# Kernel tuning notes

Hardware: AMD Instinct MI355X
Metric: run time of the kernel (lower is better)

## Reference

```python
import jax, jax.numpy as jnp
import numpy as np

K = 9          # temporal window (kernel_size)
PAD = (K - 1) // 2
BN_EPS = 1e-5


def setup_inputs() -> dict:
    key = jax.random.key(0)
    ks = jax.random.split(key, 9)
    N, Cin, Cout, T, V = 16, 64, 128, 256, 25
    return {
        "x": jax.random.normal(ks[0], (N, Cin, T, V), jnp.float32),
        "conv_w": jax.random.normal(ks[1], (Cout, Cin), jnp.float32) * (1.0 / np.sqrt(Cin)),
        "conv_b": jax.random.normal(ks[2], (Cout,), jnp.float32) * 0.01,
        "gamma": jax.random.uniform(ks[3], (Cout,), jnp.float32, 0.5, 1.5),
        "beta": jax.random.normal(ks[4], (Cout,), jnp.float32) * 0.1,
        "run_mean": jax.random.normal(ks[5], (Cout,), jnp.float32) * 0.1,
        "run_var": jax.random.uniform(ks[6], (Cout,), jnp.float32, 0.5, 1.5),
        "att0": jnp.full((1, Cout, 1, K), 1.0 / K, jnp.float32),
        "A": jax.random.uniform(ks[7], (V, V), jnp.float32),
        "keep_prob": 1,
    }


def reference(x, conv_w, conv_b, gamma, beta, run_mean, run_var, att0, A, keep_prob):
    # 1x1 conv (pointwise channel mix); AvgPool2d((1,1)) is identity for stride=1
    x = jnp.einsum("nctv,oc->notv", x, conv_w) + conv_b[None, :, None, None]
    # BatchNorm2d (eval mode: running stats)
    scale = gamma / jnp.sqrt(run_var + BN_EPS)
    x = x * scale[None, :, None, None] + (beta - run_mean * scale)[None, :, None, None]
    N, C, T, V = x.shape
    # UnfoldTemporalWindows: zero-pad T, gather K temporal shifts -> (N, C, T, K, V)
    xp = jnp.pad(x, ((0, 0), (0, 0), (PAD, PAD), (0, 0)))
    upfold = jnp.stack([xp[:, :, u:u + T, :] for u in range(K)], axis=3)
    # local attention: score each window position against the center frame
    scores = jnp.einsum("nctv,nctuv->nctu", x, upfold) / V
    attn = jax.nn.softmax(scores, axis=-1) + att0
    out = jnp.einsum("nctuv,nctu->nctv", upfold, attn)
    # dropS / dropT are identity at keep_prob == 1 (inference)
    return out
```

## Files before the change

kernel.cpp:

```cpp
#include <hip/hip_runtime.h>
#include <hip/hip_bf16.h>

#define CIN   64
#define COUT  128
#define TT    256
#define VV    25
#define TV    (TT * VV)
#define KW    9
#define PAD   4
#define RSF   32

typedef __attribute__((ext_vector_type(8))) short short8;
typedef __attribute__((ext_vector_type(4))) float f32x4;

__device__ __forceinline__ unsigned f2b(float f) {
    unsigned u = __builtin_bit_cast(unsigned, f);
    return (u + 0x7FFFu + ((u >> 16) & 1u)) >> 16;
}
__device__ __forceinline__ float b2f(unsigned short u) {
    unsigned v = (unsigned)u << 16;
    return __builtin_bit_cast(float, v);
}
__device__ __forceinline__ int swz(int row, int cbyte) {
    return row * 128 + ((cbyte & ~15) ^ ((row & 7) << 4)) + (cbyte & 15);
}
__device__ __forceinline__ int aswz(int t, int v) {
    return t * RSF + ((((v >> 2) ^ ((t >> 1) & 7))) << 2) + (v & 3);
}
__device__ __forceinline__ const float4* arow(const float* yl, int r, int k) {
    return (const float4*)&yl[r * RSF + ((k ^ ((r >> 1) & 7)) << 2)];
}

__global__ __launch_bounds__(256) void conv_mfma(
    const float* __restrict__ x, const float* __restrict__ w,
    const float* __restrict__ cb, const float* __restrict__ gamma,
    const float* __restrict__ beta, const float* __restrict__ rm,
    const float* __restrict__ rv, unsigned short* __restrict__ y)
{
    __shared__ __align__(16) unsigned short Wl[COUT * 64];
    __shared__ __align__(16) unsigned short Xl[128 * 64];
    __shared__ float sc[COUT];
    __shared__ float of[COUT];

    const int pc  = blockIdx.x;
    const int n   = blockIdx.y;
    const int tid = threadIdx.x;
    const int posbase = pc * 128;

    if (tid < COUT) {
        const float s = gamma[tid] * rsqrtf(rv[tid] + 1e-5f);
        sc[tid] = s;
        of[tid] = cb[tid] * s + beta[tid] - rm[tid] * s;
    }
    for (int idx = tid; idx < 2048; idx += 256) {
        const int c4 = idx & 15, o = idx >> 4;
        const f32x4 wv = *(const f32x4*)(w + o * 64 + c4 * 4);
        uint2 pk;
        pk.x = f2b(wv.x) | (f2b(wv.y) << 16);
        pk.y = f2b(wv.z) | (f2b(wv.w) << 16);
        *(uint2*)((char*)Wl + swz(o, c4 * 8)) = pk;
    }
    for (int idx = tid; idx < 2048; idx += 256) {
        const int pos = idx & 127, c4 = idx >> 7;
        const float* xp = x + (size_t)n * CIN * TV + (size_t)(c4 * 4) * TV + posbase + pos;
        const float a0 = xp[0], a1 = xp[TV], a2 = xp[2 * TV], a3 = xp[3 * TV];
        uint2 pk;
        pk.x = f2b(a0) | (f2b(a1) << 16);
        pk.y = f2b(a2) | (f2b(a3) << 16);
        *(uint2*)((char*)Xl + swz(pos, c4 * 8)) = pk;
    }
    __syncthreads();

    const int wv_ = tid >> 6, lane = tid & 63;
    const int lr = lane & 15, lh = lane >> 4;

    short8 afr[2][2];
#pragma unroll
    for (int m0 = 0; m0 < 2; ++m0)
#pragma unroll
        for (int kh = 0; kh < 2; ++kh)
            afr[m0][kh] = *(const short8*)((const char*)Wl +
                              swz(wv_ * 32 + m0 * 16 + lr, kh * 64 + lh * 16));

    f32x4 acc[2][8];
#pragma unroll
    for (int m0 = 0; m0 < 2; ++m0)
#pragma unroll
        for (int n0 = 0; n0 < 8; ++n0) acc[m0][n0] = (f32x4){0.f, 0.f, 0.f, 0.f};

#pragma unroll
    for (int n0 = 0; n0 < 8; ++n0) {
        const int prow = n0 * 16 + lr;
        const short8 b0 = *(const short8*)((const char*)Xl + swz(prow, lh * 16));
        const short8 b1 = *(const short8*)((const char*)Xl + swz(prow, 64 + lh * 16));
#pragma unroll
        for (int m0 = 0; m0 < 2; ++m0) {
            acc[m0][n0] = __builtin_amdgcn_mfma_f32_16x16x32_bf16(afr[m0][0], b0, acc[m0][n0], 0, 0, 0);
            acc[m0][n0] = __builtin_amdgcn_mfma_f32_16x16x32_bf16(afr[m0][1], b1, acc[m0][n0], 0, 0, 0);
        }
    }

    unsigned short* yb = y + (size_t)n * COUT * TV + posbase;
#pragma unroll
    for (int m0 = 0; m0 < 2; ++m0)
#pragma unroll
        for (int n0 = 0; n0 < 8; ++n0)
#pragma unroll
            for (int r = 0; r < 4; ++r) {
                const int o = wv_ * 32 + m0 * 16 + lh * 4 + r;
                const int pos = n0 * 16 + lr;
                const float val = acc[m0][n0][r] * sc[o] + of[o];
                yb[(size_t)o * TV + pos] = (unsigned short)f2b(val);
            }
}

__global__ __launch_bounds__(128) void attn_kernel(
    const unsigned short* __restrict__ y, const float* __restrict__ att0,
    float* __restrict__ out)
{
    __shared__ float yl[TT * RSF];
    __shared__ float a0s[KW];

    const int nc  = blockIdx.x;
    const int c   = nc & (COUT - 1);
    const int tid = threadIdx.x;

    const unsigned short* yp = y + (size_t)nc * TV;

    for (int j = tid; j < TT * 7; j += 128) {
        const int t = j / 7, p = j - t * 7;
        yl[aswz(t, 25 + p)] = 0.f;
    }
    for (int i = tid; i < TV / 4; i += 128) {
        const ushort4 u = *(const ushort4*)(yp + i * 4);
        const int e = i * 4;
        const float f[4] = { b2f(u.x), b2f(u.y), b2f(u.z), b2f(u.w) };
#pragma unroll
        for (int j = 0; j < 4; ++j) {
            const int t = (e + j) / 25, v = (e + j) % 25;
            yl[aswz(t, v)] = f[j];
        }
    }
    if (tid < KW) a0s[tid] = att0[c * KW + tid];
    __syncthreads();

    const int t0 = tid * 2, t1 = t0 + 1;

    float4 yc0[7], yc1[7];
#pragma unroll
    for (int k = 0; k < 7; ++k) { yc0[k] = *arow(yl, t0, k); yc1[k] = *arow(yl, t1, k); }

    float s0[KW], s1[KW];
#pragma unroll
    for (int u = 0; u < KW; ++u) { s0[u] = 0.f; s1[u] = 0.f; }

#pragma unroll
    for (int j = 0; j < 10; ++j) {
        const int r = t0 - PAD + j;
        if (r >= 0 && r < TT) {
            float d0 = 0.f, d1 = 0.f;
#pragma unroll
            for (int k = 0; k < 7; ++k) {
                const float4 q = *arow(yl, r, k);
                d0 = fmaf(q.x, yc0[k].x, d0); d0 = fmaf(q.y, yc0[k].y, d0);
                d0 = fmaf(q.z, yc0[k].z, d0); d0 = fmaf(q.w, yc0[k].w, d0);
                d1 = fmaf(q.x, yc1[k].x, d1); d1 = fmaf(q.y, yc1[k].y, d1);
                d1 = fmaf(q.z, yc1[k].z, d1); d1 = fmaf(q.w, yc1[k].w, d1);
            }
            if (j <= 8) s0[j]     = d0 * (1.f / (float)VV);
            if (j >= 1) s1[j - 1] = d1 * (1.f / (float)VV);
        }
    }

    float aw0[KW], aw1[KW];
    {
        float m0 = s0[0], m1 = s1[0];
#pragma unroll
        for (int u = 1; u < KW; ++u) { m0 = fmaxf(m0, s0[u]); m1 = fmaxf(m1, s1[u]); }
        float d0 = 0.f, d1 = 0.f;
#pragma unroll
        for (int u = 0; u < KW; ++u) {
            aw0[u] = __expf(s0[u] - m0); d0 += aw0[u];
            aw1[u] = __expf(s1[u] - m1); d1 += aw1[u];
        }
        const float i0 = 1.f / d0, i1 = 1.f / d1;
#pragma unroll
        for (int u = 0; u < KW; ++u) {
            aw0[u] = aw0[u] * i0 + a0s[u];
            aw1[u] = aw1[u] * i1 + a0s[u];
        }
    }

    float4 o0[7], o1[7];
#pragma unroll
    for (int k = 0; k < 7; ++k) {
        o0[k] = make_float4(0.f, 0.f, 0.f, 0.f);
        o1[k] = make_float4(0.f, 0.f, 0.f, 0.f);
    }
#pragma unroll
    for (int j = 0; j < 10; ++j) {
        const int r = t0 - PAD + j;
        if (r >= 0 && r < TT) {
#pragma unroll
            for (int k = 0; k < 7; ++k) {
                const float4 q = *arow(yl, r, k);
                if (j <= 8) {
                    const float a = aw0[j];
                    o0[k].x = fmaf(a, q.x, o0[k].x); o0[k].y = fmaf(a, q.y, o0[k].y);
                    o0[k].z = fmaf(a, q.z, o0[k].z); o0[k].w = fmaf(a, q.w, o0[k].w);
                }
                if (j >= 1) {
                    const float a = aw1[j - 1];
                    o1[k].x = fmaf(a, q.x, o1[k].x); o1[k].y = fmaf(a, q.y, o1[k].y);
                    o1[k].z = fmaf(a, q.z, o1[k].z); o1[k].w = fmaf(a, q.w, o1[k].w);
                }
            }
        }
    }

    __syncthreads();
    {
        float* op0 = &yl[t0 * VV];
        float* op1 = &yl[t1 * VV];
#pragma unroll
        for (int k = 0; k < 6; ++k) {
            op0[4*k+0] = o0[k].x; op0[4*k+1] = o0[k].y; op0[4*k+2] = o0[k].z; op0[4*k+3] = o0[k].w;
            op1[4*k+0] = o1[k].x; op1[4*k+1] = o1[k].y; op1[4*k+2] = o1[k].z; op1[4*k+3] = o1[k].w;
        }
        op0[24] = o0[6].x;
        op1[24] = o1[6].x;
    }
    __syncthreads();
    {
        float4* og = (float4*)(out + (size_t)nc * TV);
        const float4* yl4 = (const float4*)yl;
        for (int i = tid; i < TV / 4; i += 128) og[i] = yl4[i];
    }
}

extern "C" void kernel_launch(void* const* d_in, const int* in_sizes, int n_in,
                              void* d_out, int out_size, void* d_ws, size_t ws_size,
                              hipStream_t stream)
{
    const float* x     = (const float*)d_in[0];
    const float* w     = (const float*)d_in[1];
    const float* cb    = (const float*)d_in[2];
    const float* gamma = (const float*)d_in[3];
    const float* beta  = (const float*)d_in[4];
    const float* rm    = (const float*)d_in[5];
    const float* rv    = (const float*)d_in[6];
    const float* att0  = (const float*)d_in[7];
    float* out = (float*)d_out;
    unsigned short* y = (unsigned short*)d_ws;

    dim3 gA(TV / 128, 16);
    conv_mfma<<<gA, 256, 0, stream>>>(x, w, cb, gamma, beta, rm, rv, y);

    dim3 gB(16 * COUT);
    attn_kernel<<<gB, 128, 0, stream>>>(y, att0, out);
}
```

Baseline: 53.13 us.

## Store intermediate in padded bf16 row layout and keep it bf16 in LDS

The conv kernel now writes its bf16 output in a padded (t, 32) row layout and zeroes the padding lanes, so the attention kernel can load each channel plane with aligned 16-byte vector loads into a swizzled bf16 LDS tile. It adds zero halo rows in LDS, which removes the boundary branches. Rows are unpacked to fp32 in registers when used. The output is stored directly to global memory from registers instead of being staged through LDS, and launch bounds request 3 blocks per CU. This halves the LDS footprint and drops the per-element div/mod scatter, at the cost of more register pressure and more scattered global stores in the conv epilogue.

```diff
diff --git a/kernel.cpp b/kernel.cpp
--- a/kernel.cpp
+++ b/kernel.cpp
@@ -8,7 +8,8 @@
 #define TV    (TT * VV)
 #define KW    9
 #define PAD   4
-#define RSF   32
+#define YROW  32
+#define YSTR  (TT * YROW)
 
 typedef __attribute__((ext_vector_type(8))) short short8;
 typedef __attribute__((ext_vector_type(4))) float f32x4;
@@ -17,18 +18,18 @@
     unsigned u = __builtin_bit_cast(unsigned, f);
     return (u + 0x7FFFu + ((u >> 16) & 1u)) >> 16;
 }
-__device__ __forceinline__ float b2f(unsigned short u) {
-    unsigned v = (unsigned)u << 16;
-    return __builtin_bit_cast(float, v);
+__device__ __forceinline__ float lof(unsigned u) {
+    return __builtin_bit_cast(float, u << 16);
+}
+__device__ __forceinline__ float hif(unsigned u) {
+    return __builtin_bit_cast(float, u & 0xffff0000u);
+}
+__device__ __forceinline__ void unpack8(uint4 u, float* d) {
+    d[0] = lof(u.x); d[1] = hif(u.x); d[2] = lof(u.y); d[3] = hif(u.y);
+    d[4] = lof(u.z); d[5] = hif(u.z); d[6] = lof(u.w); d[7] = hif(u.w);
 }
 __device__ __forceinline__ int swz(int row, int cbyte) {
     return row * 128 + ((cbyte & ~15) ^ ((row & 7) << 4)) + (cbyte & 15);
-}
-__device__ __forceinline__ int aswz(int t, int v) {
-    return t * RSF + ((((v >> 2) ^ ((t >> 1) & 7))) << 2) + (v & 3);
-}
-__device__ __forceinline__ const float4* arow(const float* yl, int r, int k) {
-    return (const float4*)&yl[r * RSF + ((k ^ ((r >> 1) & 7)) << 2)];
 }
 
 __global__ __launch_bounds__(256) void conv_mfma(
@@ -100,7 +101,7 @@
         }
     }
 
-    unsigned short* yb = y + (size_t)n * COUT * TV + posbase;
+    const size_t ybase = (size_t)(n * COUT) * YSTR;
 #pragma unroll
     for (int m0 = 0; m0 < 2; ++m0)
 #pragma unroll
@@ -108,71 +109,91 @@
 #pragma unroll
             for (int r = 0; r < 4; ++r) {
                 const int o = wv_ * 32 + m0 * 16 + lh * 4 + r;
-                const int pos = n0 * 16 + lr;
+                const int pos = posbase + n0 * 16 + lr;
+                const int t = pos / 25;
+                const int v = pos - t * 25;
                 const float val = acc[m0][n0][r] * sc[o] + of[o];
-                yb[(size_t)o * TV + pos] = (unsigned short)f2b(val);
+                y[ybase + (size_t)o * YSTR + t * YROW + v] = (unsigned short)f2b(val);
             }
-}
-
-__global__ __launch_bounds__(128) void attn_kernel(
+
+    const int tfirst = (posbase + 24) / 25;
+    for (int idx = tid; idx < 6 * 128; idx += 256) {
+        const int ri = idx >> 7;
+        const int o  = idx & 127;
+        const int t  = tfirst + ri;
+        if (25 * t < posbase + 128 && t < 256) {
+            unsigned char* pb = (unsigned char*)y + (ybase + (size_t)o * YSTR + t * YROW) * 2 + 50;
+            *(unsigned short*)(pb)     = 0;
+            *(unsigned*)(pb + 2)       = 0;
+            *(uint2*)(pb + 6)          = make_uint2(0, 0);
+        }
+    }
+}
+
+__global__ __launch_bounds__(128, 3) void attn_kernel(
     const unsigned short* __restrict__ y, const float* __restrict__ att0,
     float* __restrict__ out)
 {
-    __shared__ float yl[TT * RSF];
+    __shared__ uint4 tile[132 * 8];
     __shared__ float a0s[KW];
 
     const int nc  = blockIdx.x;
     const int c   = nc & (COUT - 1);
     const int tid = threadIdx.x;
 
-    const unsigned short* yp = y + (size_t)nc * TV;
-
-    for (int j = tid; j < TT * 7; j += 128) {
-        const int t = j / 7, p = j - t * 7;
-        yl[aswz(t, 25 + p)] = 0.f;
-    }
-    for (int i = tid; i < TV / 4; i += 128) {
-        const ushort4 u = *(const ushort4*)(yp + i * 4);
-        const int e = i * 4;
-        const float f[4] = { b2f(u.x), b2f(u.y), b2f(u.z), b2f(u.w) };
-#pragma unroll
-        for (int j = 0; j < 4; ++j) {
-            const int t = (e + j) / 25, v = (e + j) % 25;
-            yl[aswz(t, v)] = f[j];
-        }
-    }
     if (tid < KW) a0s[tid] = att0[c * KW + tid];
+
+    if (tid < 32) {
+        const int pi = tid >> 3;
+        const int p  = (pi < 2) ? pi : (128 + pi);
+        tile[p * 8 + (tid & 7)] = make_uint4(0, 0, 0, 0);
+    }
+
+    const uint4* yg = (const uint4*)(y + (size_t)nc * YSTR);
+#pragma unroll
+    for (int i = 0; i < 8; ++i) {
+        const int ci = tid + i * 128;
+        const int sp = 2 + (ci >> 3);
+        const int h8 = (ci & 7) ^ (sp & 7);
+        const int r  = ((sp - 2) << 1) | (h8 >> 2);
+        const int q  = h8 & 3;
+        tile[16 + ci] = yg[r * 4 + q];
+    }
     __syncthreads();
 
-    const int t0 = tid * 2, t1 = t0 + 1;
-
-    float4 yc0[7], yc1[7];
-#pragma unroll
-    for (int k = 0; k < 7; ++k) { yc0[k] = *arow(yl, t0, k); yc1[k] = *arow(yl, t1, k); }
+    const int t0 = tid * 2;
+
+#define LOADROW(rp, dst)                                                   \
+    {                                                                      \
+        const int s_ = (rp) >> 1, e_ = s_ & 7, hb_ = ((rp) & 1) << 2;      \
+        const uint4 u0 = tile[s_ * 8 + ((hb_ | 0) ^ e_)];                  \
+        const uint4 u1 = tile[s_ * 8 + ((hb_ | 1) ^ e_)];                  \
+        const uint4 u2 = tile[s_ * 8 + ((hb_ | 2) ^ e_)];                  \
+        const uint4 u3 = tile[s_ * 8 + ((hb_ | 3) ^ e_)];                  \
+        unpack8(u0, (dst) + 0); unpack8(u1, (dst) + 8);                    \
+        unpack8(u2, (dst) + 16); (dst)[24] = lof(u3.x);                    \
+    }
+
+    float q0[25], q1[25];
+    LOADROW(t0 + 4, q0);
+    LOADROW(t0 + 5, q1);
 
     float s0[KW], s1[KW];
 #pragma unroll
-    for (int u = 0; u < KW; ++u) { s0[u] = 0.f; s1[u] = 0.f; }
-
-#pragma unroll
     for (int j = 0; j < 10; ++j) {
-        const int r = t0 - PAD + j;
-        if (r >= 0 && r < TT) {
-            float d0 = 0.f, d1 = 0.f;
-#pragma unroll
-            for (int k = 0; k < 7; ++k) {
-                const float4 q = *arow(yl, r, k);
-                d0 = fmaf(q.x, yc0[k].x, d0); d0 = fmaf(q.y, yc0[k].y, d0);
-                d0 = fmaf(q.z, yc0[k].z, d0); d0 = fmaf(q.w, yc0[k].w, d0);
-                d1 = fmaf(q.x, yc1[k].x, d1); d1 = fmaf(q.y, yc1[k].y, d1);
-                d1 = fmaf(q.z, yc1[k].z, d1); d1 = fmaf(q.w, yc1[k].w, d1);
-            }
-            if (j <= 8) s0[j]     = d0 * (1.f / (float)VV);
-            if (j >= 1) s1[j - 1] = d1 * (1.f / (float)VV);
-        }
-    }
-
-    float aw0[KW], aw1[KW];
+        const int rp = t0 + j;
+        float row[25];
+        LOADROW(rp, row);
+        float d0 = 0.f, d1 = 0.f;
+#pragma unroll
+        for (int v = 0; v < 25; ++v) {
+            d0 = fmaf(row[v], q0[v], d0);
+            d1 = fmaf(row[v], q1[v], d1);
+        }
+        if (j <= 8) s0[j]     = d0 * (1.0f / 25.0f);
+        if (j >= 1) s1[j - 1] = d1 * (1.0f / 25.0f);
+    }
+
     {
         float m0 = s0[0], m1 = s1[0];
 #pragma unroll
@@ -180,62 +201,47 @@
         float d0 = 0.f, d1 = 0.f;
 #pragma unroll
         for (int u = 0; u < KW; ++u) {
-            aw0[u] = __expf(s0[u] - m0); d0 += aw0[u];
-            aw1[u] = __expf(s1[u] - m1); d1 += aw1[u];
+            s0[u] = __expf(s0[u] - m0); d0 += s0[u];
+            s1[u] = __expf(s1[u] - m1); d1 += s1[u];
         }
         const float i0 = 1.f / d0, i1 = 1.f / d1;
 #pragma unroll
         for (int u = 0; u < KW; ++u) {
-            aw0[u] = aw0[u] * i0 + a0s[u];
-            aw1[u] = aw1[u] * i1 + a0s[u];
-        }
-    }
-
-    float4 o0[7], o1[7];
-#pragma unroll
-    for (int k = 0; k < 7; ++k) {
-        o0[k] = make_float4(0.f, 0.f, 0.f, 0.f);
-        o1[k] = make_float4(0.f, 0.f, 0.f, 0.f);
-    }
+            s0[u] = s0[u] * i0 + a0s[u];
+            s1[u] = s1[u] * i1 + a0s[u];
+        }
+    }
+
+    float o0[25], o1[25];
+#pragma unroll
+    for (int v = 0; v < 25; ++v) { o0[v] = 0.f; o1[v] = 0.f; }
 #pragma unroll
     for (int j = 0; j < 10; ++j) {
-        const int r = t0 - PAD + j;
-        if (r >= 0 && r < TT) {
-#pragma unroll
-            for (int k = 0; k < 7; ++k) {
-                const float4 q = *arow(yl, r, k);
-                if (j <= 8) {
-                    const float a = aw0[j];
-                    o0[k].x = fmaf(a, q.x, o0[k].x); o0[k].y = fmaf(a, q.y, o0[k].y);
-                    o0[k].z = fmaf(a, q.z, o0[k].z); o0[k].w = fmaf(a, q.w, o0[k].w);
-                }
-                if (j >= 1) {
-                    const float a = aw1[j - 1];
-                    o1[k].x = fmaf(a, q.x, o1[k].x); o1[k].y = fmaf(a, q.y, o1[k].y);
-                    o1[k].z = fmaf(a, q.z, o1[k].z); o1[k].w = fmaf(a, q.w, o1[k].w);
-                }
-            }
-        }
-    }
-
-    __syncthreads();
-    {
-        float* op0 = &yl[t0 * VV];
-        float* op1 = &yl[t1 * VV];
-#pragma unroll
-        for (int k = 0; k < 6; ++k) {
-            op0[4*k+0] = o0[k].x; op0[4*k+1] = o0[k].y; op0[4*k+2] = o0[k].z; op0[4*k+3] = o0[k].w;
-            op1[4*k+0] = o1[k].x; op1[4*k+1] = o1[k].y; op1[4*k+2] = o1[k].z; op1[4*k+3] = o1[k].w;
-        }
-        op0[24] = o0[6].x;
-        op1[24] = o1[6].x;
-    }
-    __syncthreads();
-    {
-        float4* og = (float4*)(out + (size_t)nc * TV);
-        const float4* yl4 = (const float4*)yl;
-        for (int i = tid; i < TV / 4; i += 128) og[i] = yl4[i];
-    }
+        const int rp = t0 + j;
+        float row[25];
+        LOADROW(rp, row);
+        if (j <= 8) {
+            const float a = s0[j];
+#pragma unroll
+            for (int v = 0; v < 25; ++v) o0[v] = fmaf(a, row[v], o0[v]);
+        }
+        if (j >= 1) {
+            const float a = s1[j - 1];
+#pragma unroll
+            for (int v = 0; v < 25; ++v) o1[v] = fmaf(a, row[v], o1[v]);
+        }
+    }
+#undef LOADROW
+
+    float* p0 = out + (size_t)nc * TV + t0 * 25;
+    float* p1 = p0 + 25;
+#pragma unroll
+    for (int k = 0; k < 12; ++k) {
+        *(float2*)(p0 + 2 * k) = make_float2(o0[2 * k], o0[2 * k + 1]);
+        *(float2*)(p1 + 2 * k) = make_float2(o1[2 * k], o1[2 * k + 1]);
+    }
+    p0[24] = o0[24];
+    p1[24] = o1[24];
 }
 
 extern "C" void kernel_launch(void* const* d_in, const int* in_sizes, int n_in,
```

New measurement: 182.8 us. 244% more time.
